# Performance work log

Hardware: AMD Instinct MI355X
Metric: run time of the kernel (lower is better)

The kernel has to match this reference:

```python
import jax, jax.numpy as jnp
import numpy as np

B, T, C, H = 4, 4096, 1024, 64

def setup_inputs() -> dict:
    key = jax.random.key(0)
    kx, kk, kq, kv = jax.random.split(key, 4)
    x = jax.random.normal(kx, (B, T, C), dtype=jnp.float32)
    Wk = jax.random.normal(kk, (C, H), dtype=jnp.float32) * (C ** -0.5)
    Wq = jax.random.normal(kq, (C, H), dtype=jnp.float32) * (C ** -0.5)
    Wv = jax.random.normal(kv, (C, H), dtype=jnp.float32) * (C ** -0.5)
    return {"x": x, "Wk": Wk, "Wq": Wq, "Wv": Wv}

def reference(x, Wk, Wq, Wv):
    Bb, Tt, Cc = x.shape
    k = jnp.einsum('btc,ch->bth', x, Wk)
    q = jnp.einsum('btc,ch->bth', x, Wq)
    v = jnp.einsum('btc,ch->bth', x, Wv)
    # NOTE: source scales by C**-0.5 with C = embed dim (not head_size)
    scores = jnp.einsum('bqh,bkh->bqk', q, k) * (Cc ** -0.5)
    causal = jnp.tril(jnp.ones((Tt, Tt), dtype=bool))
    scores = jnp.where(causal, scores, -jnp.inf)
    weights = jax.nn.softmax(scores, axis=-1)
    out = jnp.einsum('bqk,bkh->bqh', weights, v)
    return out
```

## Files before the change

kernel.cpp:

```cpp
#include <hip/hip_runtime.h>
#include <hip/hip_bf16.h>

typedef _Float16 f16x8 __attribute__((ext_vector_type(8)));
typedef _Float16 f16x4 __attribute__((ext_vector_type(4)));
typedef __fp16 fp16x2 __attribute__((ext_vector_type(2)));
typedef float f32x4 __attribute__((ext_vector_type(4)));

#define BATCH 4
#define SEQ 4096
#define EMB 1024
#define HEAD 64

__device__ __forceinline__ void async_copy16(const void* gsrc, void* ldst) {
  __builtin_amdgcn_global_load_lds(
      (const __attribute__((address_space(1))) void*)gsrc,
      (__attribute__((address_space(3))) void*)ldst,
      16, 0, 0);
}

__global__ __launch_bounds__(256) void wtrans_kernel(
    const float* __restrict__ Wk, const float* __restrict__ Wq,
    const float* __restrict__ Wv, _Float16* __restrict__ WT) {
  int id = blockIdx.x * 256 + threadIdx.x;
  int step = id / 1536;
  int rem = id - step * 1536;
  int G = rem / 192;
  int n = rem - G * 192;
  int sel = n >> 6;
  int col = n & 63;
  const float* src = (sel == 0) ? Wq : (sel == 1) ? Wk : Wv;
  const float scale = (sel == 0) ? 0.03125f : 1.0f;
  f16x8 u;
#pragma unroll
  for (int j = 0; j < 8; ++j) {
    int k = step * 64 + G * 8 + j;
    u[j] = (_Float16)(src[k * 64 + col] * scale);
  }
  *(f16x8*)(WT + (size_t)id * 8) = u;
}

__global__ __launch_bounds__(256) void proj_kernel(
    const float* __restrict__ x, const _Float16* __restrict__ WT,
    _Float16* __restrict__ Qh, _Float16* __restrict__ KT,
    _Float16* __restrict__ VT) {
  __shared__ _Float16 wtl[2][12288];
  __shared__ float xls[3][32 * 64];
  const int tid = threadIdx.x;
  const int wave = tid >> 6;
  const int lane = tid & 63;
  const int quad = lane >> 4;
  const int l16 = lane & 15;
  const int wm = wave & 1;
  const int wn = wave >> 1;
  const int rowblk = blockIdx.x * 32;

  const int lq = lane >> 4;
  const int pos = lane & 15;

  f32x4 acc[6];
#pragma unroll
  for (int t = 0; t < 6; ++t) acc[t] = (f32x4){0.f, 0.f, 0.f, 0.f};

#pragma unroll
  for (int i = 0; i < 6; ++i) {
    const int c = wave * 6 + i;
    async_copy16(WT + (size_t)c * 512 + lane * 8, (char*)&wtl[0][0] + c * 1024);
  }
#pragma unroll
  for (int i = 0; i < 2; ++i) {
    const int c = wave * 2 + i;
    const int rts = c * 4 + lq;
    const int u = pos ^ (rts & 7);
    async_copy16(x + (size_t)(rowblk + rts) * EMB + u * 4,
                 (char*)&xls[0][0] + c * 1024);
  }
#pragma unroll
  for (int i = 0; i < 2; ++i) {
    const int c = wave * 2 + i;
    const int rts = c * 4 + lq;
    const int u = pos ^ (rts & 7);
    async_copy16(x + (size_t)(rowblk + rts) * EMB + 64 + u * 4,
                 (char*)&xls[1][0] + c * 1024);
  }

  const int rt = wm * 16 + l16;
  const int rb = rt & 7;
  const int ua = ((quad * 2) ^ rb) * 4;
  const int ub = ((quad * 2 + 1) ^ rb) * 4;
  const int uc = ((8 + quad * 2) ^ rb) * 4;
  const int ud = ((8 + quad * 2 + 1) ^ rb) * 4;

  int pw = 0;
  int x3 = 0;
  int x3i = 2;
  for (int step = 0; step < 16; ++step) {
    if (step < 15) {
      asm volatile("s_waitcnt vmcnt(2)" ::: "memory");
    } else {
      asm volatile("s_waitcnt vmcnt(0)" ::: "memory");
    }
    __builtin_amdgcn_sched_barrier(0);
    __builtin_amdgcn_s_barrier();

    if (step + 1 < 16) {
      const _Float16* wsrc = WT + (size_t)(step + 1) * 12288;
#pragma unroll
      for (int i = 0; i < 6; ++i) {
        const int c = wave * 6 + i;
        async_copy16(wsrc + (size_t)c * 512 + lane * 8,
                     (char*)&wtl[pw ^ 1][0] + c * 1024);
      }
    }
    if (step + 2 < 16) {
      const float* xsrc = x + (size_t)(step + 2) * 64;
#pragma unroll
      for (int i = 0; i < 2; ++i) {
        const int c = wave * 2 + i;
        const int rts = c * 4 + lq;
        const int u = pos ^ (rts & 7);
        async_copy16(xsrc + (size_t)(rowblk + rts) * EMB + u * 4,
                     (char*)&xls[x3i][0] + c * 1024);
      }
    }

    const float* xl = &xls[x3][rt * 64];
    const float4 xa = *(const float4*)(xl + ua);
    const float4 xb = *(const float4*)(xl + ub);
    const float4 xc = *(const float4*)(xl + uc);
    const float4 xd = *(const float4*)(xl + ud);
    fp16x2 p0 = __builtin_amdgcn_cvt_pkrtz(xa.x, xa.y);
    fp16x2 p1 = __builtin_amdgcn_cvt_pkrtz(xa.z, xa.w);
    fp16x2 p2 = __builtin_amdgcn_cvt_pkrtz(xb.x, xb.y);
    fp16x2 p3 = __builtin_amdgcn_cvt_pkrtz(xb.z, xb.w);
    f16x8 af0, af1;
    af0[0] = (_Float16)p0[0]; af0[1] = (_Float16)p0[1];
    af0[2] = (_Float16)p1[0]; af0[3] = (_Float16)p1[1];
    af0[4] = (_Float16)p2[0]; af0[5] = (_Float16)p2[1];
    af0[6] = (_Float16)p3[0]; af0[7] = (_Float16)p3[1];
    p0 = __builtin_amdgcn_cvt_pkrtz(xc.x, xc.y);
    p1 = __builtin_amdgcn_cvt_pkrtz(xc.z, xc.w);
    p2 = __builtin_amdgcn_cvt_pkrtz(xd.x, xd.y);
    p3 = __builtin_amdgcn_cvt_pkrtz(xd.z, xd.w);
    af1[0] = (_Float16)p0[0]; af1[1] = (_Float16)p0[1];
    af1[2] = (_Float16)p1[0]; af1[3] = (_Float16)p1[1];
    af1[4] = (_Float16)p2[0]; af1[5] = (_Float16)p2[1];
    af1[6] = (_Float16)p3[0]; af1[7] = (_Float16)p3[1];
#pragma unroll
    for (int t = 0; t < 6; ++t) {
      const int n = wn * 96 + t * 16 + l16;
      const f16x8 b0 = *(const f16x8*)&wtl[pw][(size_t)((0 * 4 + quad) * 192 + n) * 8];
      const f16x8 b1 = *(const f16x8*)&wtl[pw][(size_t)((1 * 4 + quad) * 192 + n) * 8];
      acc[t] = __builtin_amdgcn_mfma_f32_16x16x32_f16(af0, b0, acc[t], 0, 0, 0);
      acc[t] = __builtin_amdgcn_mfma_f32_16x16x32_f16(af1, b1, acc[t], 0, 0, 0);
    }
    pw ^= 1;
    x3 = (x3 == 2) ? 0 : x3 + 1;
    x3i = (x3i == 2) ? 0 : x3i + 1;
  }

  const int rowbase = rowblk + wm * 16;
  const int b = rowbase >> 12;
  const int trbase = (rowbase & 4095) + quad * 4;
#pragma unroll
  for (int t = 0; t < 6; ++t) {
    const int g = wn * 6 + t;
    if (g < 4) {
      const int h = g * 16 + l16;
#pragma unroll
      for (int r = 0; r < 4; ++r)
        Qh[(size_t)(rowbase + quad * 4 + r) * HEAD + h] = (_Float16)acc[t][r];
    } else if (g < 8) {
      const int h = (g - 4) * 16 + l16;
#pragma unroll
      for (int r = 0; r < 4; ++r) {
        const int t0 = trbase + r;
        const size_t ad = ((size_t)((b * 64 + (t0 >> 6)) * 8 + (h >> 3)) * 64 +
                           (t0 & 63)) * 8 + (h & 7);
        KT[ad] = (_Float16)acc[t][r];
      }
    } else {
      const int h = (g - 8) * 16 + l16;
      f16x4 pk;
      pk[0] = (_Float16)acc[t][0]; pk[1] = (_Float16)acc[t][1];
      pk[2] = (_Float16)acc[t][2]; pk[3] = (_Float16)acc[t][3];
      const size_t ad = ((size_t)((b * 64 + (trbase >> 6)) * 8 + ((trbase & 63) >> 3)) * 512) +
                        (size_t)h * 8 + (trbase & 7);
      *(f16x4*)(VT + ad) = pk;
    }
  }
}

__global__ __launch_bounds__(256) void flash_kernel(
    const _Float16* __restrict__ Qh, const _Float16* __restrict__ KT,
    const _Float16* __restrict__ VT, float* __restrict__ out) {
  __shared__ _Float16 myp[4][16 * 68];
  __shared__ float lds_o[2][16][68];
  __shared__ float lds_l[2][16];
  const int tid = threadIdx.x;
  const int w = tid >> 6;
  const int lane = tid & 63;
  const int quad = lane >> 4;
  const int l16 = lane & 15;
  const int b = blockIdx.x & 3;
  const int jj = blockIdx.x >> 2;
  const int t = w >> 1;
  const int kh = w & 1;
  const int j = t ? (255 - jj) : jj;
  const int qb = j * 16;
  const int nkt = (j >> 2) + 1;
  const int h1 = (nkt + 1) >> 1;
  const int lo = kh ? h1 : 0;
  const int hi = kh ? nkt : h1;

  const _Float16* Q = Qh + (size_t)b * SEQ * HEAD;
  const _Float16* KTb = KT + (size_t)b * 64 * 4096;
  const _Float16* VTb = VT + (size_t)b * 64 * 4096;
  const f32x4 zero = {0.f, 0.f, 0.f, 0.f};
  _Float16* mp = &myp[w][0];

  const f16x8 aq0 = *(const f16x8*)(Q + (size_t)(qb + l16) * HEAD + quad * 8);
  const f16x8 aq1 = *(const f16x8*)(Q + (size_t)(qb + l16) * HEAD + 32 + quad * 8);
  const int qrow = qb + quad * 4;

  f32x4 oc[4];
#pragma unroll
  for (int m = 0; m < 4; ++m) oc[m] = zero;
  float lacc[4] = {0.f, 0.f, 0.f, 0.f};

  f16x8 ka[4], kb[4];
  if (lo < hi) {
    const _Float16* kp = KTb + (size_t)lo * 4096;
#pragma unroll
    for (int s = 0; s < 4; ++s) {
      ka[s] = *(const f16x8*)(kp + (size_t)quad * 512 + (s * 16 + l16) * 8);
      kb[s] = *(const f16x8*)(kp + (size_t)(4 + quad) * 512 + (s * 16 + l16) * 8);
    }
  }

  for (int kt = lo; kt < hi; ++kt) {
    const _Float16* vp = VTb + (size_t)kt * 4096;
    f16x8 va[4], vb[4];
#pragma unroll
    for (int m = 0; m < 4; ++m) {
      va[m] = *(const f16x8*)(vp + (size_t)quad * 512 + (m * 16 + l16) * 8);
      vb[m] = *(const f16x8*)(vp + (size_t)(4 + quad) * 512 + (m * 16 + l16) * 8);
    }

    f32x4 sc[4];
#pragma unroll
    for (int s = 0; s < 4; ++s) {
      sc[s] = __builtin_amdgcn_mfma_f32_16x16x32_f16(aq0, ka[s], zero, 0, 0, 0);
      sc[s] = __builtin_amdgcn_mfma_f32_16x16x32_f16(aq1, kb[s], sc[s], 0, 0, 0);
    }

    if (kt + 1 < hi) {
      const _Float16* kp = KTb + (size_t)(kt + 1) * 4096;
#pragma unroll
      for (int s = 0; s < 4; ++s) {
        ka[s] = *(const f16x8*)(kp + (size_t)quad * 512 + (s * 16 + l16) * 8);
        kb[s] = *(const f16x8*)(kp + (size_t)(4 + quad) * 512 + (s * 16 + l16) * 8);
      }
    }

    const int kbase = kt * 64;
    if (kt == nkt - 1) {
#pragma unroll
      for (int s = 0; s < 4; ++s) {
#pragma unroll
        for (int r = 0; r < 4; ++r) {
          const float pv = (kbase + s * 16 + l16 > qrow + r) ? 0.f : __expf(sc[s][r]);
          lacc[r] += pv;
          mp[(quad * 4 + r) * 68 + s * 16 + l16] = (_Float16)pv;
        }
      }
    } else {
#pragma unroll
      for (int s = 0; s < 4; ++s) {
#pragma unroll
        for (int r = 0; r < 4; ++r) {
          const float pv = __expf(sc[s][r]);
          lacc[r] += pv;
          mp[(quad * 4 + r) * 68 + s * 16 + l16] = (_Float16)pv;
        }
      }
    }

    const f16x8 ap0 = *(const f16x8*)(mp + l16 * 68 + quad * 8);
    const f16x8 ap1 = *(const f16x8*)(mp + l16 * 68 + 32 + quad * 8);

#pragma unroll
    for (int m = 0; m < 4; ++m) {
      oc[m] = __builtin_amdgcn_mfma_f32_16x16x32_f16(ap0, va[m], oc[m], 0, 0, 0);
      oc[m] = __builtin_amdgcn_mfma_f32_16x16x32_f16(ap1, vb[m], oc[m], 0, 0, 0);
    }
  }

  float lr[4];
#pragma unroll
  for (int r = 0; r < 4; ++r) {
    float l = lacc[r];
    l += __shfl_xor(l, 1);
    l += __shfl_xor(l, 2);
    l += __shfl_xor(l, 4);
    l += __shfl_xor(l, 8);
    lr[r] = l;
  }

  if (kh) {
#pragma unroll
    for (int r = 0; r < 4; ++r) {
      if (l16 == 0) lds_l[t][quad * 4 + r] = lr[r];
#pragma unroll
      for (int m = 0; m < 4; ++m)
        lds_o[t][quad * 4 + r][m * 16 + l16] = oc[m][r];
    }
  }
  __syncthreads();
  if (!kh) {
#pragma unroll
    for (int r = 0; r < 4; ++r) {
      const float lsum = lr[r] + lds_l[t][quad * 4 + r];
      const float inv = 1.0f / lsum;
      float* op = out + ((size_t)b * SEQ + qb + quad * 4 + r) * HEAD + l16;
#pragma unroll
      for (int m = 0; m < 4; ++m)
        op[m * 16] = (oc[m][r] + lds_o[t][quad * 4 + r][m * 16 + l16]) * inv;
    }
  }
}

extern "C" void kernel_launch(void* const* d_in, const int* in_sizes, int n_in,
                              void* d_out, int out_size, void* d_ws, size_t ws_size,
                              hipStream_t stream) {
  const float* x  = (const float*)d_in[0];
  const float* Wk = (const float*)d_in[1];
  const float* Wq = (const float*)d_in[2];
  const float* Wv = (const float*)d_in[3];
  float* out = (float*)d_out;

  char* ws = (char*)d_ws;
  _Float16* Qh = (_Float16*)(ws);
  _Float16* KT = (_Float16*)(ws + (size_t)2 * 1024 * 1024);
  _Float16* VT = (_Float16*)(ws + (size_t)4 * 1024 * 1024);
  _Float16* WT = (_Float16*)(ws + (size_t)6 * 1024 * 1024);

  wtrans_kernel<<<96, 256, 0, stream>>>(Wk, Wq, Wv, WT);
  proj_kernel<<<512, 256, 0, stream>>>(x, WT, Qh, KT, VT);
  flash_kernel<<<512, 256, 0, stream>>>(Qh, KT, VT, out);
}
```

Measured before the change: 137.6 us.

## Process 32 query rows per wave and split KV range across four waves

The flash kernel now handles 32-row query tiles per wave, so two 16-row sub-tiles share each loaded K/V fragment. The key range is split four ways instead of two across the waves of a 512-thread block. Partial outputs are combined through LDS by all waves, with vectorized float4 stores. The aim is to halve K/V global loads per query row and improve load balance, at the cost of more registers and LDS per block and a four-way reduction.

```diff
diff --git a/kernel.cpp b/kernel.cpp
--- a/kernel.cpp
+++ b/kernel.cpp
@@ -190,12 +190,12 @@
   }
 }
 
-__global__ __launch_bounds__(256) void flash_kernel(
+__global__ __launch_bounds__(512) void flash_kernel(
     const _Float16* __restrict__ Qh, const _Float16* __restrict__ KT,
     const _Float16* __restrict__ VT, float* __restrict__ out) {
-  __shared__ _Float16 myp[4][16 * 68];
-  __shared__ float lds_o[2][16][68];
-  __shared__ float lds_l[2][16];
+  __shared__ _Float16 myp[8][32 * 68];
+  __shared__ float lds_o[2][4][32][68];
+  __shared__ float lds_l[2][4][32];
   const int tid = threadIdx.x;
   const int w = tid >> 6;
   const int lane = tid & 63;
@@ -203,14 +203,13 @@
   const int l16 = lane & 15;
   const int b = blockIdx.x & 3;
   const int jj = blockIdx.x >> 2;
-  const int t = w >> 1;
-  const int kh = w & 1;
-  const int j = t ? (255 - jj) : jj;
-  const int qb = j * 16;
-  const int nkt = (j >> 2) + 1;
-  const int h1 = (nkt + 1) >> 1;
-  const int lo = kh ? h1 : 0;
-  const int hi = kh ? nkt : h1;
+  const int t = w >> 2;
+  const int q = w & 3;
+  const int j = t ? (127 - jj) : jj;
+  const int qb = j * 32;
+  const int nkt = (j >> 1) + 1;
+  const int lo = (nkt * q) >> 2;
+  const int hi = (nkt * (q + 1)) >> 2;
 
   const _Float16* Q = Qh + (size_t)b * SEQ * HEAD;
   const _Float16* KTb = KT + (size_t)b * 64 * 4096;
@@ -218,14 +217,19 @@
   const f32x4 zero = {0.f, 0.f, 0.f, 0.f};
   _Float16* mp = &myp[w][0];
 
-  const f16x8 aq0 = *(const f16x8*)(Q + (size_t)(qb + l16) * HEAD + quad * 8);
-  const f16x8 aq1 = *(const f16x8*)(Q + (size_t)(qb + l16) * HEAD + 32 + quad * 8);
-  const int qrow = qb + quad * 4;
-
-  f32x4 oc[4];
-#pragma unroll
-  for (int m = 0; m < 4; ++m) oc[m] = zero;
-  float lacc[4] = {0.f, 0.f, 0.f, 0.f};
+  f16x8 aq0[2], aq1[2];
+#pragma unroll
+  for (int rt = 0; rt < 2; ++rt) {
+    aq0[rt] = *(const f16x8*)(Q + (size_t)(qb + rt * 16 + l16) * HEAD + quad * 8);
+    aq1[rt] = *(const f16x8*)(Q + (size_t)(qb + rt * 16 + l16) * HEAD + 32 + quad * 8);
+  }
+
+  f32x4 oc[2][4];
+#pragma unroll
+  for (int rt = 0; rt < 2; ++rt)
+#pragma unroll
+    for (int m = 0; m < 4; ++m) oc[rt][m] = zero;
+  float lacc[2][4] = {{0.f, 0.f, 0.f, 0.f}, {0.f, 0.f, 0.f, 0.f}};
 
   f16x8 ka[4], kb[4];
   if (lo < hi) {
@@ -246,11 +250,14 @@
       vb[m] = *(const f16x8*)(vp + (size_t)(4 + quad) * 512 + (m * 16 + l16) * 8);
     }
 
-    f32x4 sc[4];
+    f32x4 sc[2][4];
 #pragma unroll
     for (int s = 0; s < 4; ++s) {
-      sc[s] = __builtin_amdgcn_mfma_f32_16x16x32_f16(aq0, ka[s], zero, 0, 0, 0);
-      sc[s] = __builtin_amdgcn_mfma_f32_16x16x32_f16(aq1, kb[s], sc[s], 0, 0, 0);
+#pragma unroll
+      for (int rt = 0; rt < 2; ++rt) {
+        sc[rt][s] = __builtin_amdgcn_mfma_f32_16x16x32_f16(aq0[rt], ka[s], zero, 0, 0, 0);
+        sc[rt][s] = __builtin_amdgcn_mfma_f32_16x16x32_f16(aq1[rt], kb[s], sc[rt][s], 0, 0, 0);
+      }
     }
 
     if (kt + 1 < hi) {
@@ -265,67 +272,81 @@
     const int kbase = kt * 64;
     if (kt == nkt - 1) {
 #pragma unroll
-      for (int s = 0; s < 4; ++s) {
-#pragma unroll
-        for (int r = 0; r < 4; ++r) {
-          const float pv = (kbase + s * 16 + l16 > qrow + r) ? 0.f : __expf(sc[s][r]);
-          lacc[r] += pv;
-          mp[(quad * 4 + r) * 68 + s * 16 + l16] = (_Float16)pv;
+      for (int rt = 0; rt < 2; ++rt) {
+        const int qrow = qb + rt * 16 + quad * 4;
+#pragma unroll
+        for (int s = 0; s < 4; ++s) {
+#pragma unroll
+          for (int r = 0; r < 4; ++r) {
+            const float pv = (kbase + s * 16 + l16 > qrow + r) ? 0.f : __expf(sc[rt][s][r]);
+            lacc[rt][r] += pv;
+            mp[(rt * 16 + quad * 4 + r) * 68 + s * 16 + l16] = (_Float16)pv;
+          }
         }
       }
     } else {
 #pragma unroll
-      for (int s = 0; s < 4; ++s) {
-#pragma unroll
-        for (int r = 0; r < 4; ++r) {
-          const float pv = __expf(sc[s][r]);
-          lacc[r] += pv;
-          mp[(quad * 4 + r) * 68 + s * 16 + l16] = (_Float16)pv;
+      for (int rt = 0; rt < 2; ++rt) {
+#pragma unroll
+        for (int s = 0; s < 4; ++s) {
+#pragma unroll
+          for (int r = 0; r < 4; ++r) {
+            const float pv = __expf(sc[rt][s][r]);
+            lacc[rt][r] += pv;
+            mp[(rt * 16 + quad * 4 + r) * 68 + s * 16 + l16] = (_Float16)pv;
+          }
         }
       }
     }
 
-    const f16x8 ap0 = *(const f16x8*)(mp + l16 * 68 + quad * 8);
-    const f16x8 ap1 = *(const f16x8*)(mp + l16 * 68 + 32 + quad * 8);
-
-#pragma unroll
-    for (int m = 0; m < 4; ++m) {
-      oc[m] = __builtin_amdgcn_mfma_f32_16x16x32_f16(ap0, va[m], oc[m], 0, 0, 0);
-      oc[m] = __builtin_amdgcn_mfma_f32_16x16x32_f16(ap1, vb[m], oc[m], 0, 0, 0);
-    }
-  }
-
-  float lr[4];
-#pragma unroll
-  for (int r = 0; r < 4; ++r) {
-    float l = lacc[r];
-    l += __shfl_xor(l, 1);
-    l += __shfl_xor(l, 2);
-    l += __shfl_xor(l, 4);
-    l += __shfl_xor(l, 8);
-    lr[r] = l;
-  }
-
-  if (kh) {
+#pragma unroll
+    for (int rt = 0; rt < 2; ++rt) {
+      const f16x8 ap0 = *(const f16x8*)(mp + (rt * 16 + l16) * 68 + quad * 8);
+      const f16x8 ap1 = *(const f16x8*)(mp + (rt * 16 + l16) * 68 + 32 + quad * 8);
+#pragma unroll
+      for (int m = 0; m < 4; ++m) {
+        oc[rt][m] = __builtin_amdgcn_mfma_f32_16x16x32_f16(ap0, va[m], oc[rt][m], 0, 0, 0);
+        oc[rt][m] = __builtin_amdgcn_mfma_f32_16x16x32_f16(ap1, vb[m], oc[rt][m], 0, 0, 0);
+      }
+    }
+  }
+
+#pragma unroll
+  for (int rt = 0; rt < 2; ++rt) {
 #pragma unroll
     for (int r = 0; r < 4; ++r) {
-      if (l16 == 0) lds_l[t][quad * 4 + r] = lr[r];
+      float l = lacc[rt][r];
+      l += __shfl_xor(l, 1);
+      l += __shfl_xor(l, 2);
+      l += __shfl_xor(l, 4);
+      l += __shfl_xor(l, 8);
+      const int row = rt * 16 + quad * 4 + r;
+      if (l16 == 0) lds_l[t][q][row] = l;
 #pragma unroll
       for (int m = 0; m < 4; ++m)
-        lds_o[t][quad * 4 + r][m * 16 + l16] = oc[m][r];
+        lds_o[t][q][row][m * 16 + l16] = oc[rt][m][r];
     }
   }
   __syncthreads();
-  if (!kh) {
-#pragma unroll
-    for (int r = 0; r < 4; ++r) {
-      const float lsum = lr[r] + lds_l[t][quad * 4 + r];
-      const float inv = 1.0f / lsum;
-      float* op = out + ((size_t)b * SEQ + qb + quad * 4 + r) * HEAD + l16;
-#pragma unroll
-      for (int m = 0; m < 4; ++m)
-        op[m * 16] = (oc[m][r] + lds_o[t][quad * 4 + r][m * 16 + l16]) * inv;
-    }
+
+  {
+    const int row = q * 8 + (lane >> 3);
+    const int h8 = (lane & 7) * 8;
+    const int jt = t ? (127 - jj) : jj;
+    const float lsum = lds_l[t][0][row] + lds_l[t][1][row] +
+                       lds_l[t][2][row] + lds_l[t][3][row];
+    const float inv = 1.0f / lsum;
+    float4 o0, o1;
+#pragma unroll
+    for (int i = 0; i < 4; ++i) {
+      ((float*)&o0)[i] = (lds_o[t][0][row][h8 + i] + lds_o[t][1][row][h8 + i] +
+                          lds_o[t][2][row][h8 + i] + lds_o[t][3][row][h8 + i]) * inv;
+      ((float*)&o1)[i] = (lds_o[t][0][row][h8 + 4 + i] + lds_o[t][1][row][h8 + 4 + i] +
+                          lds_o[t][2][row][h8 + 4 + i] + lds_o[t][3][row][h8 + 4 + i]) * inv;
+    }
+    float* op = out + ((size_t)b * SEQ + jt * 32 + row) * HEAD + h8;
+    *(float4*)op = o0;
+    *(float4*)(op + 4) = o1;
   }
 }
 
@@ -346,5 +367,5 @@
 
   wtrans_kernel<<<96, 256, 0, stream>>>(Wk, Wq, Wv, WT);
   proj_kernel<<<512, 256, 0, stream>>>(x, WT, Qh, KT, VT);
-  flash_kernel<<<512, 256, 0, stream>>>(Qh, KT, VT, out);
-}
+  flash_kernel<<<256, 512, 0, stream>>>(Qh, KT, VT, out);
+}
```

After: 135.7 us. About the same (-1.4%).
